# Kernel tuning notes

Hardware: AMD Instinct MI355X
Metric: run time of the kernel (lower is better)

Reference implementation:

```python
import jax, jax.numpy as jnp
from jax import lax
import numpy as np

EPS = 1e-6

def layer_norm(x, scale, bias):
    mu = jnp.mean(x, axis=-1, keepdims=True)
    var = jnp.var(x, axis=-1, keepdims=True)
    y = (x - mu) * lax.rsqrt(var + EPS)
    if scale is not None:
        y = y * scale
    if bias is not None:
        y = y + bias
    return y

def mha(keys, values, queries, mask, head_count):
    # keys/values: [B, K, E]; queries: [B, Q, E]; mask: [B, K] (1 = attend)
    B, Q, E = queries.shape
    d = E // head_count
    q = queries.reshape(B, Q, head_count, d) / jnp.asarray(d ** 0.5, queries.dtype)
    k = keys.reshape(B, -1, head_count, d)
    v = values.reshape(B, -1, head_count, d)
    bias = (1.0 - mask.astype(q.dtype)) * -1e12  # [B, K]
    w = jnp.einsum('bqhc,bkhc->bhqk', q, k) + bias[:, None, None, :]
    w = jax.nn.softmax(w, axis=-1)
    out = jnp.einsum('bhqk,bkhc->bqhc', w, v)
    return out.reshape(B, Q, E)

def setup_inputs() -> dict:
    key = jax.random.key(0)
    ks = jax.random.split(key, 16)
    B, T, E, G, I = 64, 64, 2048, 4096, 256
    s = 0.02
    inp = {
        'decoder_state': jax.random.normal(ks[0], (B, 1, E), jnp.float32),
        'encoder_state': jax.random.normal(ks[1], (B, T, E), jnp.float32),
        'attention_state': jnp.zeros((2 * B, I, E), jnp.float32),
        'attention_mask': jnp.ones((B, T), jnp.int32),
        'token_index': 100,
        # params
        'ln_pre_sa_b': jnp.zeros((E,), jnp.float32),
        'q_sa': s * jax.random.normal(ks[2], (E, E), jnp.float32),
        'k_sa': s * jax.random.normal(ks[3], (E, E), jnp.float32),
        'v_sa': s * jax.random.normal(ks[4], (E, E), jnp.float32),
        'o_sa': s * jax.random.normal(ks[5], (E, E), jnp.float32),
        'ln_sa_s': jnp.ones((E,), jnp.float32),
        'ln_sa_b': jnp.zeros((E,), jnp.float32),
        'ln_pre_ca_b': jnp.zeros((E,), jnp.float32),
        'q_ca': s * jax.random.normal(ks[6], (E, E), jnp.float32),
        'k_ca': s * jax.random.normal(ks[7], (E, E), jnp.float32),
        'v_ca': s * jax.random.normal(ks[8], (E, E), jnp.float32),
        'o_ca': s * jax.random.normal(ks[9], (E, E), jnp.float32),
        'ln_ca_s': jnp.ones((E,), jnp.float32),
        'ln_ca_b': jnp.zeros((E,), jnp.float32),
        'glu_ln0_b': jnp.zeros((E,), jnp.float32),
        'fc0_w': s * jax.random.normal(ks[10], (E, G), jnp.float32),
        'fc1_w': s * jax.random.normal(ks[11], (E, G), jnp.float32),
        'glu_ln1_s': jnp.ones((G,), jnp.float32),
        'glu_ln1_b': jnp.zeros((G,), jnp.float32),
        'fc2_w': s * jax.random.normal(ks[12], (G, E), jnp.float32),
    }
    return inp

IMAGE_TOKEN_COUNT = 256
HEAD_COUNT = 32

def reference(decoder_state, encoder_state, attention_state,
              ln_pre_sa_b, q_sa, k_sa, v_sa, o_sa, ln_sa_s, ln_sa_b,
              ln_pre_ca_b, q_ca, k_ca, v_ca, o_ca, ln_ca_s, ln_ca_b,
              glu_ln0_b, fc0_w, fc1_w, glu_ln1_s, glu_ln1_b, fc2_w,
              attention_mask, token_index):
    B = decoder_state.shape[0]
    # --- self attention (pre-norm, KV cache update) ---
    residual = decoder_state
    x = layer_norm(decoder_state, None, ln_pre_sa_b)
    self_mask = jnp.tile(jnp.arange(IMAGE_TOKEN_COUNT) < token_index + 1, (B, 1))
    keys = x @ k_sa
    values = x @ v_sa
    queries = x @ q_sa
    attention_state = lax.dynamic_update_slice(
        attention_state, jnp.concatenate([keys, values]).astype(jnp.float32),
        (0, token_index, 0))
    cached_k = attention_state[:B]
    cached_v = attention_state[B:]
    x = (mha(cached_k, cached_v, queries, self_mask, HEAD_COUNT) @ o_sa).astype(decoder_state.dtype)
    x = layer_norm(x, ln_sa_s, ln_sa_b)
    decoder_state = residual + x
    # --- cross attention ---
    residual = decoder_state
    x = layer_norm(decoder_state, None, ln_pre_ca_b)
    ek = encoder_state @ k_ca
    ev = encoder_state @ v_ca
    q = x @ q_ca
    x = mha(ek, ev, q, attention_mask, HEAD_COUNT) @ o_ca
    x = layer_norm(x, ln_ca_s, ln_ca_b)
    decoder_state = residual + x
    # --- GLU FFN ---
    residual = decoder_state
    z = layer_norm(decoder_state, None, glu_ln0_b)
    w = jax.nn.gelu(z @ fc0_w, approximate=False)
    v = z @ fc1_w
    z = layer_norm(w * v, glu_ln1_s, glu_ln1_b) @ fc2_w
    decoder_state = residual + z
    return decoder_state, attention_state
```

## Files before the change

kernel.cpp:

```cpp
#include <hip/hip_runtime.h>

#define Bb   64
#define Ee   2048
#define Tt   64
#define Gg   4096
#define Ii   256
#define Hh   32
#define Dd   64

using f32x4_t  = __attribute__((ext_vector_type(4))) float;

__device__ __forceinline__ float gelu_f(float x) {
  return 0.5f * x * (1.0f + erff(x * 0.70710678118654752f));
}

__global__ void copy_state_k(const float4* __restrict__ src, float4* __restrict__ dst,
                             const float4* __restrict__ kb, const float4* __restrict__ vb,
                             const int* __restrict__ tokp) {
  const int t = *tokp;
  const long n4 = (long)128 * Ii * (Ee / 4);
  long i = (long)blockIdx.x * blockDim.x + threadIdx.x;
  const long stride = (long)gridDim.x * blockDim.x;
  for (; i < n4; i += stride) {
    long row = i >> 9;
    int tt = (int)(row & (Ii - 1));
    float4 v;
    if (tt == t) {
      int bh  = (int)(row >> 8);
      int col = (int)(i & 511);
      const float4* s = (bh < Bb) ? kb : vb;
      v = s[(long)(bh & (Bb - 1)) * (Ee / 4) + col];
    } else {
      v = src[i];
    }
    dst[i] = v;
  }
}

template <bool GELU, bool HAS_SCALE, bool HAS_RES, bool DUAL>
__global__ void ln_k(const float4* __restrict__ in1, const float4* __restrict__ in2,
                     const float* __restrict__ scale, const float* __restrict__ bias,
                     const float4* __restrict__ res,
                     float4* __restrict__ out1, float4* __restrict__ out2) {
  const int row = blockIdx.x, tid = threadIdx.x;
  const int C = blockDim.x * 4;
  const long base = (long)row * blockDim.x + tid;

  float4 p = in1[base];
  if (GELU) {
    float4 vv = in2[base];
    p.x = gelu_f(p.x) * vv.x; p.y = gelu_f(p.y) * vv.y;
    p.z = gelu_f(p.z) * vv.z; p.w = gelu_f(p.w) * vv.w;
  }
  float s  = p.x + p.y + p.z + p.w;
  float s2 = p.x * p.x + p.y * p.y + p.z * p.z + p.w * p.w;

  __shared__ float rs[16], rs2[16];
  int lane = tid & 63, w = tid >> 6;
  #pragma unroll
  for (int o = 32; o; o >>= 1) { s += __shfl_down(s, o, 64); s2 += __shfl_down(s2, o, 64); }
  if (lane == 0) { rs[w] = s; rs2[w] = s2; }
  __syncthreads();
  if (tid == 0) {
    float ts = 0.f, ts2 = 0.f;
    int nw = blockDim.x >> 6;
    for (int i = 0; i < nw; i++) { ts += rs[i]; ts2 += rs2[i]; }
    float mu = ts / C;
    float var = ts2 / C - mu * mu;
    rs[0]  = mu;
    rs2[0] = rsqrtf(var + 1e-6f);
  }
  __syncthreads();
  const float mu = rs[0], rstd = rs2[0];

  float4 o;
  o.x = (p.x - mu) * rstd; o.y = (p.y - mu) * rstd;
  o.z = (p.z - mu) * rstd; o.w = (p.w - mu) * rstd;
  if (HAS_SCALE) {
    float4 sc4 = ((const float4*)scale)[tid];
    o.x *= sc4.x; o.y *= sc4.y; o.z *= sc4.z; o.w *= sc4.w;
  }
  float4 b4 = ((const float4*)bias)[tid];
  o.x += b4.x; o.y += b4.y; o.z += b4.z; o.w += b4.w;
  if (HAS_RES) {
    float4 r4 = res[base];
    o.x += r4.x; o.y += r4.y; o.z += r4.z; o.w += r4.w;
  }
  out1[base] = o;
  if (DUAL) out2[base] = o;
}

template <int NW>
__global__ __launch_bounds__(256)
void proj_k(const float* __restrict__ X,
            const float* __restrict__ W0, const float* __restrict__ W1,
            const float* __restrict__ W2,
            float* __restrict__ P, int K, int N) {
  __shared__ float Xs[64 * 64];
  const int nq = threadIdx.x & 31;
  const int m0 = (threadIdx.x >> 5) * 8;
  const int n  = blockIdx.x * 128 + nq * 4;
  const int kbase = blockIdx.y * 128;

  f32x4_t acc[NW][8];
  #pragma unroll
  for (int wsel = 0; wsel < NW; wsel++)
    #pragma unroll
    for (int i = 0; i < 8; i++) acc[wsel][i] = (f32x4_t){0.f, 0.f, 0.f, 0.f};

  for (int k0 = kbase; k0 < kbase + 128; k0 += 64) {
    __syncthreads();
    #pragma unroll
    for (int j = 0; j < 16; j++) {
      int e = threadIdx.x + j * 256;
      Xs[e] = X[(long)(e >> 6) * K + k0 + (e & 63)];
    }
    __syncthreads();
    #pragma unroll 4
    for (int kk = 0; kk < 64; kk++) {
      const long wrow = (long)(k0 + kk) * N + n;
      f32x4_t w4[NW];
      w4[0] = *(const f32x4_t*)(W0 + wrow);
      if (NW > 1) w4[1] = *(const f32x4_t*)(W1 + wrow);
      if (NW > 2) w4[2] = *(const f32x4_t*)(W2 + wrow);
      #pragma unroll
      for (int i = 0; i < 8; i++) {
        float xm = Xs[(m0 + i) * 64 + kk];
        #pragma unroll
        for (int wsel = 0; wsel < NW; wsel++) acc[wsel][i] += xm * w4[wsel];
      }
    }
  }
  float* base = P + (long)blockIdx.y * ((long)NW * 64 * N);
  #pragma unroll
  for (int wsel = 0; wsel < NW; wsel++) {
    #pragma unroll
    for (int i = 0; i < 8; i++) {
      *(f32x4_t*)(base + ((long)wsel * 64 + m0 + i) * N + n) = acc[wsel][i];
    }
  }
}

template <bool ACCUM>
__global__ void reduce_k(const float4* __restrict__ P, float4* __restrict__ Y,
                         int KB, long n4) {
  long i = (long)blockIdx.x * blockDim.x + threadIdx.x;
  if (i >= n4) return;
  float4 s = ACCUM ? Y[i] : make_float4(0.f, 0.f, 0.f, 0.f);
  for (int k = 0; k < KB; k++) {
    float4 p = P[(long)k * n4 + i];
    s.x += p.x; s.y += p.y; s.z += p.z; s.w += p.w;
  }
  Y[i] = s;
}

__global__ void attn_k(const float* __restrict__ Q, const float* __restrict__ Kc,
                       const float* __restrict__ Vc, float* __restrict__ O,
                       const int* __restrict__ tokp, int L, long bstride, float scale) {
  const int b = blockIdx.x, h = blockIdx.y;
  const int lane = threadIdx.x;
  __shared__ float sc[256];
  const float* qp = Q + (long)b * Ee + h * Dd;
  const int n = *tokp + 1;

  float mx = -3.0e38f;
  for (int pos = lane; pos < n; pos += 64) {
    const float* kr = Kc + (long)b * bstride + (long)pos * Ee + h * Dd;
    float acc = 0.f;
    #pragma unroll
    for (int j = 0; j < 16; j++) {
      float4 kv = *(const float4*)(kr + j * 4);
      acc += qp[j*4+0]*kv.x + qp[j*4+1]*kv.y + qp[j*4+2]*kv.z + qp[j*4+3]*kv.w;
    }
    float s = acc * scale;
    sc[pos] = s;
    mx = fmaxf(mx, s);
  }
  __syncthreads();
  #pragma unroll
  for (int o = 32; o; o >>= 1) mx = fmaxf(mx, __shfl_down(mx, o, 64));
  mx = __shfl(mx, 0, 64);

  float sum = 0.f;
  for (int pos = lane; pos < n; pos += 64) {
    float e = expf(sc[pos] - mx);
    sc[pos] = e;
    sum += e;
  }
  __syncthreads();
  #pragma unroll
  for (int o = 32; o; o >>= 1) sum += __shfl_down(sum, o, 64);
  sum = __shfl(sum, 0, 64);
  const float inv = 1.0f / sum;

  const float* vbase = Vc + (long)b * bstride + h * Dd + lane;
  float acc = 0.f;
  int pos = 0;
  for (; pos + 8 <= n; pos += 8) {
    #pragma unroll
    for (int u = 0; u < 8; u++)
      acc += sc[pos + u] * vbase[(long)(pos + u) * Ee];
  }
  for (; pos < n; pos++) acc += sc[pos] * vbase[(long)pos * Ee];
  O[(long)b * Ee + h * Dd + lane] = acc * inv;
}


__global__ __launch_bounds__(256)
void headA_k(const float* __restrict__ Q, const float* __restrict__ Kca,
             float* __restrict__ A) {
  const int h  = blockIdx.x;
  const int e0 = blockIdx.y * 128;
  __shared__ float Qs[64][64];
  __shared__ float Kt[64][132];
  const int tid = threadIdx.x;

  #pragma unroll
  for (int j = 0; j < 16; j++) {
    int idx = tid + j * 256;
    Qs[idx >> 6][idx & 63] = Q[(long)(idx >> 6) * Ee + h * 64 + (idx & 63)];
  }
  #pragma unroll
  for (int j = 0; j < 32; j++) {
    int idx = tid + j * 256;
    int r = idx >> 6, c = idx & 63;
    Kt[c][r] = Kca[(long)(e0 + r) * Ee + h * 64 + c];
  }
  __syncthreads();

  const int nq = tid & 31, m0 = (tid >> 5) * 8;
  f32x4_t acc[8];
  #pragma unroll
  for (int i = 0; i < 8; i++) acc[i] = (f32x4_t){0.f, 0.f, 0.f, 0.f};
  #pragma unroll 8
  for (int c = 0; c < 64; c++) {
    f32x4_t w4 = *(const f32x4_t*)&Kt[c][nq * 4];
    #pragma unroll
    for (int i = 0; i < 8; i++) acc[i] += Qs[m0 + i][c] * w4;
  }
  #pragma unroll
  for (int i = 0; i < 8; i++)
    *(f32x4_t*)&A[((long)(m0 + i) * Hh + h) * Ee + e0 + nq * 4] = acc[i] * 0.125f;
}

__global__ __launch_bounds__(256)
void sm_k(const float* __restrict__ A, const float* __restrict__ enc,
          const int* __restrict__ mask, float* __restrict__ P) {
  const int b = blockIdx.x, hg = blockIdx.y;
  __shared__ float Es[64][65];
  __shared__ float As[8][64];
  const int tid = threadIdx.x;
  const int t = tid & 63, h2 = tid >> 6;

  float s0 = 0.f, s1 = 0.f;
  for (int e0 = 0; e0 < Ee; e0 += 64) {
    __syncthreads();
    #pragma unroll
    for (int j = 0; j < 16; j++) {
      int idx = tid + j * 256;
      Es[idx >> 6][idx & 63] = enc[((long)b * Tt + (idx >> 6)) * Ee + e0 + (idx & 63)];
    }
    #pragma unroll
    for (int j = 0; j < 2; j++) {
      int idx = tid + j * 256;
      As[idx >> 6][idx & 63] =
          A[((long)b * Hh + hg * 8 + (idx >> 6)) * Ee + e0 + (idx & 63)];
    }
    __syncthreads();
    #pragma unroll 8
    for (int e = 0; e < 64; e++) {
      float es = Es[t][e];
      s0 += As[h2][e] * es;
      s1 += As[h2 + 4][e] * es;
    }
  }

  if (mask[(long)b * Tt + t] == 0) { s0 = -1e30f; s1 = -1e30f; }
  float m0v = s0, m1v = s1;
  #pragma unroll
  for (int o = 32; o; o >>= 1) {
    m0v = fmaxf(m0v, __shfl_xor(m0v, o, 64));
    m1v = fmaxf(m1v, __shfl_xor(m1v, o, 64));
  }
  float p0 = expf(s0 - m0v), p1 = expf(s1 - m1v);
  float d0 = p0, d1 = p1;
  #pragma unroll
  for (int o = 32; o; o >>= 1) {
    d0 += __shfl_xor(d0, o, 64);
    d1 += __shfl_xor(d1, o, 64);
  }
  P[((long)b * Hh + hg * 8 + h2) * Tt + t]     = p0 / d0;
  P[((long)b * Hh + hg * 8 + h2 + 4) * Tt + t] = p1 / d1;
}

__global__ __launch_bounds__(256)
void ctxB_k(const float* __restrict__ P, const float* __restrict__ enc,
            float* __restrict__ C) {
  const int b = blockIdx.x, e0 = blockIdx.y * 256;
  __shared__ float Ps[32][64];
  const int tid = threadIdx.x;
  #pragma unroll
  for (int j = 0; j < 8; j++) {
    int idx = tid + j * 256;
    Ps[idx >> 6][idx & 63] = P[(long)b * (Hh * Tt) + idx];
  }
  __syncthreads();

  float acc[32];
  #pragma unroll
  for (int h = 0; h < 32; h++) acc[h] = 0.f;
  const float* ep = enc + (long)b * Tt * Ee + e0 + tid;
  for (int t0 = 0; t0 < Tt; t0 += 4) {
    float ev0 = ep[(long)(t0 + 0) * Ee];
    float ev1 = ep[(long)(t0 + 1) * Ee];
    float ev2 = ep[(long)(t0 + 2) * Ee];
    float ev3 = ep[(long)(t0 + 3) * Ee];
    #pragma unroll
    for (int h = 0; h < 32; h++) {
      f32x4_t p4 = *(const f32x4_t*)&Ps[h][t0];
      acc[h] += p4[0] * ev0 + p4[1] * ev1 + p4[2] * ev2 + p4[3] * ev3;
    }
  }
  #pragma unroll
  for (int h = 0; h < 32; h++)
    C[((long)b * Hh + h) * Ee + e0 + tid] = acc[h];
}

__global__ __launch_bounds__(256)
void ctxC_k(const float* __restrict__ C, const float* __restrict__ Vca,
            float* __restrict__ Pout) {
  const int h  = blockIdx.x;
  const int kb = blockIdx.y;
  __shared__ float Xs[64][65];
  __shared__ float Ws[64][64];
  const int tid = threadIdx.x;
  const int nq = tid & 15, m0 = (tid >> 4) * 4;

  f32x4_t acc[4];
  #pragma unroll
  for (int i = 0; i < 4; i++) acc[i] = (f32x4_t){0.f, 0.f, 0.f, 0.f};

  for (int k0 = kb * 512; k0 < kb * 512 + 512; k0 += 64) {
    __syncthreads();
    #pragma unroll
    for (int j = 0; j < 16; j++) {
      int idx = tid + j * 256;
      int r = idx >> 6, cc = idx & 63;
      Xs[r][cc] = C[((long)r * Hh + h) * Ee + k0 + cc];
      Ws[r][cc] = Vca[(long)(k0 + r) * Ee + h * 64 + cc];
    }
    __syncthreads();
    #pragma unroll 4
    for (int kk = 0; kk < 64; kk++) {
      f32x4_t w4 = *(const f32x4_t*)&Ws[kk][nq * 4];
      #pragma unroll
      for (int i = 0; i < 4; i++) acc[i] += Xs[m0 + i][kk] * w4;
    }
  }
  #pragma unroll
  for (int i = 0; i < 4; i++)
    *(f32x4_t*)&Pout[((long)kb * 64 + m0 + i) * Ee + h * 64 + nq * 4] = acc[i];
}

extern "C" void kernel_launch(void* const* d_in, const int* in_sizes, int n_in,
                              void* d_out, int out_size, void* d_ws, size_t ws_size,
                              hipStream_t stream) {
  const float* dec    = (const float*)d_in[0];
  const float* enc    = (const float*)d_in[1];
  const float* astate = (const float*)d_in[2];
  const int*   amask  = (const int*)d_in[3];
  const int*   tokp   = (const int*)d_in[4];
  const float* ln_pre_sa_b = (const float*)d_in[5];
  const float* q_sa = (const float*)d_in[6];
  const float* k_sa = (const float*)d_in[7];
  const float* v_sa = (const float*)d_in[8];
  const float* o_sa = (const float*)d_in[9];
  const float* ln_sa_s = (const float*)d_in[10];
  const float* ln_sa_b = (const float*)d_in[11];
  const float* ln_pre_ca_b = (const float*)d_in[12];
  const float* q_ca = (const float*)d_in[13];
  const float* k_ca = (const float*)d_in[14];
  const float* v_ca = (const float*)d_in[15];
  const float* o_ca = (const float*)d_in[16];
  const float* ln_ca_s = (const float*)d_in[17];
  const float* ln_ca_b = (const float*)d_in[18];
  const float* glu_ln0_b = (const float*)d_in[19];
  const float* fc0 = (const float*)d_in[20];
  const float* fc1 = (const float*)d_in[21];
  const float* glu_ln1_s = (const float*)d_in[22];
  const float* glu_ln1_b = (const float*)d_in[23];
  const float* fc2 = (const float*)d_in[24];

  float* out_dec   = (float*)d_out;
  float* out_state = out_dec + (long)Bb * Ee;

  float* qb  = (float*)d_ws;
  float* kb  = qb  + 131072;
  float* vb  = kb  + 131072;
  float* ob  = vb  + 131072;
  float* q2  = ob  + 131072;
  float* ob2 = q2  + 131072;
  float* w0  = ob2 + 131072;
  float* v1  = w0  + 262144;
  float* x1  = v1  + 262144;
  float* ab  = x1  + 131072;
  float* ds2 = ab  + 131072;
  float* x3  = ds2 + 131072;
  float* cb  = x3  + 131072;
  float* ds3 = cb  + 131072;
  float* zb  = ds3 + 131072;
  float* wvn = zb  + 131072;
  float* Ab   = wvn + 262144;
  float* ctxb = Ab  + 4194304;
  float* Pb   = ctxb + 4194304;
  float* arena = Pb + 131072;

  ln_k<false,false,false,false><<<Bb, 512, 0, stream>>>(
      (const float4*)dec, nullptr, nullptr, ln_pre_sa_b, nullptr, (float4*)x1, nullptr);
  proj_k<3><<<dim3(16, 16), 256, 0, stream>>>(x1, q_sa, k_sa, v_sa, arena, Ee, Ee);
  reduce_k<false><<<384, 256, 0, stream>>>((const float4*)arena, (float4*)qb, 16, 98304);
  copy_state_k<<<4096, 256, 0, stream>>>((const float4*)astate, (float4*)out_state,
                                         (const float4*)kb, (const float4*)vb, tokp);
  attn_k<<<dim3(Bb, Hh), 64, 0, stream>>>(qb, out_state,
      out_state + (long)Bb * Ii * Ee, ab, tokp, Ii, (long)Ii * Ee, 0.125f);
  proj_k<1><<<dim3(16, 16), 256, 0, stream>>>(ab, o_sa, nullptr, nullptr, arena, Ee, Ee);
  reduce_k<false><<<128, 256, 0, stream>>>((const float4*)arena, (float4*)ob, 16, 32768);
  ln_k<false,true,true,false><<<Bb, 512, 0, stream>>>(
      (const float4*)ob, nullptr, ln_sa_s, ln_sa_b, (const float4*)dec, (float4*)ds2, nullptr);

  ln_k<false,false,false,false><<<Bb, 512, 0, stream>>>(
      (const float4*)ds2, nullptr, nullptr, ln_pre_ca_b, nullptr, (float4*)x3, nullptr);
  proj_k<1><<<dim3(16, 16), 256, 0, stream>>>(x3, q_ca, nullptr, nullptr, arena, Ee, Ee);
  reduce_k<false><<<128, 256, 0, stream>>>((const float4*)arena, (float4*)q2, 16, 32768);
  headA_k<<<dim3(Hh, 16), 256, 0, stream>>>(q2, k_ca, Ab);
  sm_k<<<dim3(Bb, 4), 256, 0, stream>>>(Ab, enc, amask, Pb);
  ctxB_k<<<dim3(Bb, 8), 256, 0, stream>>>(Pb, enc, ctxb);
  ctxC_k<<<dim3(Hh, 4), 256, 0, stream>>>(ctxb, v_ca, arena);
  reduce_k<false><<<128, 256, 0, stream>>>((const float4*)arena, (float4*)cb, 4, 32768);
  proj_k<1><<<dim3(16, 16), 256, 0, stream>>>(cb, o_ca, nullptr, nullptr, arena, Ee, Ee);
  reduce_k<false><<<128, 256, 0, stream>>>((const float4*)arena, (float4*)ob2, 16, 32768);
  ln_k<false,true,true,true><<<Bb, 512, 0, stream>>>(
      (const float4*)ob2, nullptr, ln_ca_s, ln_ca_b, (const float4*)ds2,
      (float4*)ds3, (float4*)out_dec);

  ln_k<false,false,false,false><<<Bb, 512, 0, stream>>>(
      (const float4*)ds3, nullptr, nullptr, glu_ln0_b, nullptr, (float4*)zb, nullptr);
  proj_k<2><<<dim3(32, 16), 256, 0, stream>>>(zb, fc0, fc1, nullptr, arena, Ee, Gg);
  reduce_k<false><<<512, 256, 0, stream>>>((const float4*)arena, (float4*)w0, 16, 131072);
  ln_k<true,true,false,false><<<Bb, 1024, 0, stream>>>(
      (const float4*)w0, (const float4*)v1, glu_ln1_s, glu_ln1_b, nullptr, (float4*)wvn, nullptr);
  proj_k<1><<<dim3(16, 32), 256, 0, stream>>>(wvn, fc2, nullptr, nullptr, arena, Gg, Ee);
  reduce_k<true><<<128, 256, 0, stream>>>((const float4*)arena, (float4*)out_dec, 32, 32768);
}
```

Before: 1.143 ms.

## Fuse split-K partial reductions into layernorm and projection loads

```diff
diff --git a/kernel.cpp b/kernel.cpp
--- a/kernel.cpp
+++ b/kernel.cpp
@@ -37,8 +37,9 @@
   }
 }
 
-template <bool GELU, bool HAS_SCALE, bool HAS_RES, bool DUAL>
+template <bool GELU, bool HAS_SCALE, bool HAS_RES, bool DUAL, int KB>
 __global__ void ln_k(const float4* __restrict__ in1, const float4* __restrict__ in2,
+                     long kstr4, long off2,
                      const float* __restrict__ scale, const float* __restrict__ bias,
                      const float4* __restrict__ res,
                      float4* __restrict__ out1, float4* __restrict__ out2) {
@@ -46,9 +47,29 @@
   const int C = blockDim.x * 4;
   const long base = (long)row * blockDim.x + tid;
 
-  float4 p = in1[base];
+  float4 p;
+  if (KB == 0) {
+    p = in1[base];
+  } else {
+    p = make_float4(0.f, 0.f, 0.f, 0.f);
+    #pragma unroll
+    for (int k = 0; k < KB; k++) {
+      float4 q = in1[(long)k * kstr4 + base];
+      p.x += q.x; p.y += q.y; p.z += q.z; p.w += q.w;
+    }
+  }
   if (GELU) {
-    float4 vv = in2[base];
+    float4 vv;
+    if (KB == 0) {
+      vv = in2[base];
+    } else {
+      vv = make_float4(0.f, 0.f, 0.f, 0.f);
+      #pragma unroll
+      for (int k = 0; k < KB; k++) {
+        float4 q = in1[(long)k * kstr4 + off2 + base];
+        vv.x += q.x; vv.y += q.y; vv.z += q.z; vv.w += q.w;
+      }
+    }
     p.x = gelu_f(p.x) * vv.x; p.y = gelu_f(p.y) * vv.y;
     p.z = gelu_f(p.z) * vv.z; p.w = gelu_f(p.w) * vv.w;
   }
@@ -90,9 +111,9 @@
   if (DUAL) out2[base] = o;
 }
 
-template <int NW>
+template <int NW, int XP>
 __global__ __launch_bounds__(256)
-void proj_k(const float* __restrict__ X,
+void proj_k(const float* __restrict__ X, long xstr,
             const float* __restrict__ W0, const float* __restrict__ W1,
             const float* __restrict__ W2,
             float* __restrict__ P, int K, int N) {
@@ -113,7 +134,13 @@
     #pragma unroll
     for (int j = 0; j < 16; j++) {
       int e = threadIdx.x + j * 256;
-      Xs[e] = X[(long)(e >> 6) * K + k0 + (e & 63)];
+      long off = (long)(e >> 6) * K + k0 + (e & 63);
+      float sx = X[off];
+      if (XP > 1) {
+        #pragma unroll
+        for (int k = 1; k < XP; k++) sx += X[(long)k * xstr + off];
+      }
+      Xs[e] = sx;
     }
     __syncthreads();
     #pragma unroll 4
@@ -243,7 +270,7 @@
     *(f32x4_t*)&A[((long)(m0 + i) * Hh + h) * Ee + e0 + nq * 4] = acc[i] * 0.125f;
 }
 
-__global__ __launch_bounds__(256)
+__global__ __launch_bounds__(512)
 void sm_k(const float* __restrict__ A, const float* __restrict__ enc,
           const int* __restrict__ mask, float* __restrict__ P) {
   const int b = blockIdx.x, hg = blockIdx.y;
@@ -252,45 +279,29 @@
   const int tid = threadIdx.x;
   const int t = tid & 63, h2 = tid >> 6;
 
-  float s0 = 0.f, s1 = 0.f;
+  float s = 0.f;
   for (int e0 = 0; e0 < Ee; e0 += 64) {
     __syncthreads();
     #pragma unroll
-    for (int j = 0; j < 16; j++) {
-      int idx = tid + j * 256;
+    for (int j = 0; j < 8; j++) {
+      int idx = tid + j * 512;
       Es[idx >> 6][idx & 63] = enc[((long)b * Tt + (idx >> 6)) * Ee + e0 + (idx & 63)];
     }
-    #pragma unroll
-    for (int j = 0; j < 2; j++) {
-      int idx = tid + j * 256;
-      As[idx >> 6][idx & 63] =
-          A[((long)b * Hh + hg * 8 + (idx >> 6)) * Ee + e0 + (idx & 63)];
-    }
+    As[h2][t] = A[((long)b * Hh + hg * 8 + h2) * Ee + e0 + t];
     __syncthreads();
     #pragma unroll 8
-    for (int e = 0; e < 64; e++) {
-      float es = Es[t][e];
-      s0 += As[h2][e] * es;
-      s1 += As[h2 + 4][e] * es;
-    }
-  }
-
-  if (mask[(long)b * Tt + t] == 0) { s0 = -1e30f; s1 = -1e30f; }
-  float m0v = s0, m1v = s1;
-  #pragma unroll
-  for (int o = 32; o; o >>= 1) {
-    m0v = fmaxf(m0v, __shfl_xor(m0v, o, 64));
-    m1v = fmaxf(m1v, __shfl_xor(m1v, o, 64));
-  }
-  float p0 = expf(s0 - m0v), p1 = expf(s1 - m1v);
-  float d0 = p0, d1 = p1;
-  #pragma unroll
-  for (int o = 32; o; o >>= 1) {
-    d0 += __shfl_xor(d0, o, 64);
-    d1 += __shfl_xor(d1, o, 64);
-  }
-  P[((long)b * Hh + hg * 8 + h2) * Tt + t]     = p0 / d0;
-  P[((long)b * Hh + hg * 8 + h2 + 4) * Tt + t] = p1 / d1;
+    for (int e = 0; e < 64; e++) s += As[h2][e] * Es[t][e];
+  }
+
+  if (mask[(long)b * Tt + t] == 0) s = -1e30f;
+  float mv = s;
+  #pragma unroll
+  for (int o = 32; o; o >>= 1) mv = fmaxf(mv, __shfl_xor(mv, o, 64));
+  float p = expf(s - mv);
+  float d = p;
+  #pragma unroll
+  for (int o = 32; o; o >>= 1) d += __shfl_xor(d, o, 64);
+  P[((long)b * Hh + hg * 8 + h2) * Tt + t] = p / d;
 }
 
 __global__ __launch_bounds__(256)
@@ -340,7 +351,7 @@
   #pragma unroll
   for (int i = 0; i < 4; i++) acc[i] = (f32x4_t){0.f, 0.f, 0.f, 0.f};
 
-  for (int k0 = kb * 512; k0 < kb * 512 + 512; k0 += 64) {
+  for (int k0 = kb * 256; k0 < kb * 256 + 256; k0 += 64) {
     __syncthreads();
     #pragma unroll
     for (int j = 0; j < 16; j++) {
@@ -397,58 +408,56 @@
   float* qb  = (float*)d_ws;
   float* kb  = qb  + 131072;
   float* vb  = kb  + 131072;
-  float* ob  = vb  + 131072;
-  float* q2  = ob  + 131072;
-  float* ob2 = q2  + 131072;
-  float* w0  = ob2 + 131072;
-  float* v1  = w0  + 262144;
-  float* x1  = v1  + 262144;
+  float* q2  = vb  + 131072;
+  float* x1  = q2  + 131072;
   float* ab  = x1  + 131072;
   float* ds2 = ab  + 131072;
   float* x3  = ds2 + 131072;
-  float* cb  = x3  + 131072;
-  float* ds3 = cb  + 131072;
+  float* ds3 = x3  + 131072;
   float* zb  = ds3 + 131072;
   float* wvn = zb  + 131072;
   float* Ab   = wvn + 262144;
   float* ctxb = Ab  + 4194304;
   float* Pb   = ctxb + 4194304;
-  float* arena = Pb + 131072;
-
-  ln_k<false,false,false,false><<<Bb, 512, 0, stream>>>(
-      (const float4*)dec, nullptr, nullptr, ln_pre_sa_b, nullptr, (float4*)x1, nullptr);
-  proj_k<3><<<dim3(16, 16), 256, 0, stream>>>(x1, q_sa, k_sa, v_sa, arena, Ee, Ee);
-  reduce_k<false><<<384, 256, 0, stream>>>((const float4*)arena, (float4*)qb, 16, 98304);
+  float* arenaA = Pb + 131072;
+  float* arenaB = arenaA + 8388608;
+
+  ln_k<false,false,false,false,0><<<Bb, 512, 0, stream>>>(
+      (const float4*)dec, nullptr, 0, 0, nullptr, ln_pre_sa_b, nullptr,
+      (float4*)x1, nullptr);
+  proj_k<3,1><<<dim3(16, 16), 256, 0, stream>>>(x1, 0, q_sa, k_sa, v_sa, arenaA, Ee, Ee);
+  reduce_k<false><<<384, 256, 0, stream>>>((const float4*)arenaA, (float4*)qb, 16, 98304);
   copy_state_k<<<4096, 256, 0, stream>>>((const float4*)astate, (float4*)out_state,
                                          (const float4*)kb, (const float4*)vb, tokp);
   attn_k<<<dim3(Bb, Hh), 64, 0, stream>>>(qb, out_state,
       out_state + (long)Bb * Ii * Ee, ab, tokp, Ii, (long)Ii * Ee, 0.125f);
-  proj_k<1><<<dim3(16, 16), 256, 0, stream>>>(ab, o_sa, nullptr, nullptr, arena, Ee, Ee);
-  reduce_k<false><<<128, 256, 0, stream>>>((const float4*)arena, (float4*)ob, 16, 32768);
-  ln_k<false,true,true,false><<<Bb, 512, 0, stream>>>(
-      (const float4*)ob, nullptr, ln_sa_s, ln_sa_b, (const float4*)dec, (float4*)ds2, nullptr);
-
-  ln_k<false,false,false,false><<<Bb, 512, 0, stream>>>(
-      (const float4*)ds2, nullptr, nullptr, ln_pre_ca_b, nullptr, (float4*)x3, nullptr);
-  proj_k<1><<<dim3(16, 16), 256, 0, stream>>>(x3, q_ca, nullptr, nullptr, arena, Ee, Ee);
-  reduce_k<false><<<128, 256, 0, stream>>>((const float4*)arena, (float4*)q2, 16, 32768);
+  proj_k<1,1><<<dim3(16, 16), 256, 0, stream>>>(ab, 0, o_sa, nullptr, nullptr, arenaA, Ee, Ee);
+  ln_k<false,true,true,false,16><<<Bb, 512, 0, stream>>>(
+      (const float4*)arenaA, nullptr, 32768, 0, ln_sa_s, ln_sa_b,
+      (const float4*)dec, (float4*)ds2, nullptr);
+
+  ln_k<false,false,false,false,0><<<Bb, 512, 0, stream>>>(
+      (const float4*)ds2, nullptr, 0, 0, nullptr, ln_pre_ca_b, nullptr,
+      (float4*)x3, nullptr);
+  proj_k<1,1><<<dim3(16, 16), 256, 0, stream>>>(x3, 0, q_ca, nullptr, nullptr, arenaA, Ee, Ee);
+  reduce_k<false><<<128, 256, 0, stream>>>((const float4*)arenaA, (float4*)q2, 16, 32768);
   headA_k<<<dim3(Hh, 16), 256, 0, stream>>>(q2, k_ca, Ab);
-  sm_k<<<dim3(Bb, 4), 256, 0, stream>>>(Ab, enc, amask, Pb);
+  sm_k<<<dim3(Bb, 4), 512, 0, stream>>>(Ab, enc, amask, Pb);
   ctxB_k<<<dim3(Bb, 8), 256, 0, stream>>>(Pb, enc, ctxb);
-  ctxC_k<<<dim3(Hh, 4), 256, 0, stream>>>(ctxb, v_ca, arena);
-  reduce_k<false><<<128, 256, 0, stream>>>((const float4*)arena, (float4*)cb, 4, 32768);
-  proj_k<1><<<dim3(16, 16), 256, 0, stream>>>(cb, o_ca, nullptr, nullptr, arena, Ee, Ee);
-  reduce_k<false><<<128, 256, 0, stream>>>((const float4*)arena, (float4*)ob2, 16, 32768);
-  ln_k<false,true,true,true><<<Bb, 512, 0, stream>>>(
-      (const float4*)ob2, nullptr, ln_ca_s, ln_ca_b, (const float4*)ds2,
-      (float4*)ds3, (float4*)out_dec);
-
-  ln_k<false,false,false,false><<<Bb, 512, 0, stream>>>(
-      (const float4*)ds3, nullptr, nullptr, glu_ln0_b, nullptr, (float4*)zb, nullptr);
-  proj_k<2><<<dim3(32, 16), 256, 0, stream>>>(zb, fc0, fc1, nullptr, arena, Ee, Gg);
-  reduce_k<false><<<512, 256, 0, stream>>>((const float4*)arena, (float4*)w0, 16, 131072);
-  ln_k<true,true,false,false><<<Bb, 1024, 0, stream>>>(
-      (const float4*)w0, (const float4*)v1, glu_ln1_s, glu_ln1_b, nullptr, (float4*)wvn, nullptr);
-  proj_k<1><<<dim3(16, 32), 256, 0, stream>>>(wvn, fc2, nullptr, nullptr, arena, Gg, Ee);
-  reduce_k<true><<<128, 256, 0, stream>>>((const float4*)arena, (float4*)out_dec, 32, 32768);
-}
+  ctxC_k<<<dim3(Hh, 8), 256, 0, stream>>>(ctxb, v_ca, arenaB);
+  proj_k<1,8><<<dim3(16, 16), 256, 0, stream>>>(arenaB, 131072, o_ca, nullptr, nullptr,
+                                                arenaA, Ee, Ee);
+  ln_k<false,true,true,true,16><<<Bb, 512, 0, stream>>>(
+      (const float4*)arenaA, nullptr, 32768, 0, ln_ca_s, ln_ca_b,
+      (const float4*)ds2, (float4*)ds3, (float4*)out_dec);
+
+  ln_k<false,false,false,false,0><<<Bb, 512, 0, stream>>>(
+      (const float4*)ds3, nullptr, 0, 0, nullptr, glu_ln0_b, nullptr,
+      (float4*)zb, nullptr);
+  proj_k<2,1><<<dim3(32, 16), 256, 0, stream>>>(zb, 0, fc0, fc1, nullptr, arenaA, Ee, Gg);
+  ln_k<true,true,false,false,16><<<Bb, 1024, 0, stream>>>(
+      (const float4*)arenaA, nullptr, 131072, 65536, glu_ln1_s, glu_ln1_b,
+      nullptr, (float4*)wvn, nullptr);
+  proj_k<1,1><<<dim3(16, 32), 256, 0, stream>>>(wvn, 0, fc2, nullptr, nullptr, arenaB, Gg, Ee);
+  reduce_k<true><<<128, 256, 0, stream>>>((const float4*)arenaB, (float4*)out_dec, 32, 32768);
+}
```

New measurement: 1.127 ms. Within noise of the previous version (-1.4%).
